# Optimization experiments

Hardware: AMD Instinct MI355X
Metric: run time of the kernel (lower is better)

## Reference

```python
import jax, jax.numpy as jnp
import numpy as np

AREA = 8  # area_size


def setup_inputs() -> dict:
    key = jax.random.key(0)
    ks = jax.random.split(key, 8)
    b, c, h, w = 4, 256, 252, 252
    cr = c // 8  # reduction=8
    return {
        "x": jax.random.normal(ks[0], (b, c, h, w), jnp.float32),
        "Wq": jax.random.normal(ks[1], (cr, c), jnp.float32) * 0.05,
        "bq": jax.random.normal(ks[2], (cr,), jnp.float32) * 0.05,
        "Wk": jax.random.normal(ks[3], (cr, c), jnp.float32) * 0.05,
        "bk": jax.random.normal(ks[4], (cr,), jnp.float32) * 0.05,
        "Wv": jax.random.normal(ks[5], (c, c), jnp.float32) * 0.05,
        "bv": jax.random.normal(ks[6], (c,), jnp.float32) * 0.05,
        "gamma": jax.random.normal(ks[7], (1,), jnp.float32) * 0.1,
    }


def _conv1x1(x, W, bias):
    # x: [b,c,h,w], W: [o,c] -> [b,o,h,w]
    return jnp.einsum('bchw,oc->bohw', x, W) + bias[None, :, None, None]


def reference(x, Wq, bq, Wk, bk, Wv, bv, gamma):
    a = AREA
    b, c, h, w = x.shape
    ph = ((h - 1) // a + 1) * a
    pw = ((w - 1) // a + 1) * a
    xp = jnp.pad(x, ((0, 0), (0, 0), (0, ph - h), (0, pw - w)))

    q = _conv1x1(xp, Wq, bq)  # [b,cr,ph,pw]
    k = _conv1x1(xp, Wk, bk)  # [b,cr,ph,pw]
    v = _conv1x1(xp, Wv, bv)  # [b,c,ph,pw]

    nh, nw = ph // a, pw // a

    def window(t):
        # [b,C,ph,pw] -> [b*nh*nw, C, a*a]
        C = t.shape[1]
        t = t.reshape(b, C, nh, a, nw, a)
        t = t.transpose(0, 2, 4, 1, 3, 5)
        return t.reshape(b * nh * nw, C, a * a)

    qw, kw, vw = window(q), window(k), window(v)

    # attn[n,i,j] = sum_c q[n,c,i] * k[n,c,j]; softmax over j
    attn = jax.nn.softmax(jnp.einsum('nci,ncj->nij', qw, kw), axis=2)
    # out[n,c,i] = sum_j v[n,c,j] * attn[i,j]
    out = jnp.einsum('ncj,nij->nci', vw, attn)

    out = out.reshape(b, nh, nw, c, a, a)
    out = out.transpose(0, 3, 1, 4, 2, 5).reshape(b, c, ph, pw)
    out = out[:, :, :h, :w]
    return gamma * out + x
```

## Files before the change

### kernel.cpp

```cpp
#include <hip/hip_runtime.h>


#define HH 252
#define WW 252
#define CC 256
#define HW (HH * WW)

typedef __attribute__((ext_vector_type(8))) short bf8;
typedef __attribute__((ext_vector_type(4))) float f32x4;

__device__ __forceinline__ short f2bf(float f) {
    union { float f; unsigned u; } v; v.f = f;
    unsigned u = v.u;
    unsigned r = (u + 0x7fffu + ((u >> 16) & 1u)) >> 16;
    return (short)r;
}

__global__ __launch_bounds__(256) void prep_weights(
        const float* __restrict__ Wq, const float* __restrict__ Wk,
        const float* __restrict__ Wv, short* __restrict__ wf) {
    int t = blockIdx.x * 256 + threadIdx.x;
    if (t >= 81920) return;
    const float* W; int off, base;
    if (t < 8192)       { W = Wq; off = t;         base = 0; }
    else if (t < 16384) { W = Wk; off = t - 8192;  base = 8192; }
    else                { W = Wv; off = t - 16384; base = 16384; }
    int j = off & 7, l = (off >> 3) & 63, tile = off >> 9;
    int kt = tile & 7, mt = tile >> 3;
    int m = mt * 16 + (l & 15);
    int k = kt * 32 + ((l >> 4) * 8) + j;
    wf[base + off] = f2bf(W[m * 256 + k]);
}

__global__ __launch_bounds__(256) void area_attn(
        const float* __restrict__ x, const short* __restrict__ wf,
        const float* __restrict__ bq, const float* __restrict__ bk,
        const float* __restrict__ bv, const float* __restrict__ gamma,
        float* __restrict__ out) {
    __shared__ short xs[64 * 264];
    __shared__ short qs[64 * 40];
    __shared__ short ks[64 * 40];
    __shared__ short ps[64 * 72];

    const int tid  = threadIdx.x;
    const int lane = tid & 63, wv = tid >> 6;
    const int l15  = lane & 15, quad = lane >> 4;

    const int bid  = blockIdx.x;
    const int xcd  = bid & 7;
    const int j    = bid >> 3;
    const int nx   = j & 31;
    const int grow = (j >> 5) * 8 + xcd;
    const int bimg = grow >> 5;
    const int ny   = grow & 31;
    const int hb = ny * 8, wb = nx * 8;
    const float* xb = x   + (size_t)bimg * CC * HW;
    float*       ob = out + (size_t)bimg * CC * HW;

    {
        int half = tid & 1, dy = (tid >> 1) & 7, cg = tid >> 4;
        int h = hb + dy;
        int w0 = wb + half * 4;
        bool inb = (h < HH) && (w0 < WW);
        const float* src = xb + (size_t)h * WW + w0;
        int p0 = dy * 8 + half * 4;
        for (int it = 0; it < 16; ++it) {
            int c = it * 16 + cg;
            float4 f;
            if (inb) f = *reinterpret_cast<const float4*>(src + (size_t)c * HW);
            else     f = make_float4(0.f, 0.f, 0.f, 0.f);
            xs[(p0 + 0) * 264 + c] = f2bf(f.x);
            xs[(p0 + 1) * 264 + c] = f2bf(f.y);
            xs[(p0 + 2) * 264 + c] = f2bf(f.z);
            xs[(p0 + 3) * 264 + c] = f2bf(f.w);
        }
    }
    __syncthreads();

    const f32x4 zero4 = {0.f, 0.f, 0.f, 0.f};

    {
        const bool isK = (wv >> 1) != 0;
        const int mt = wv & 1;
        const short* WF = wf + (isK ? 8192 : 0);
        const float* bias = isK ? bk : bq;
        f32x4 acc[4];
        for (int nt = 0; nt < 4; ++nt) acc[nt] = zero4;
        for (int kt = 0; kt < 8; ++kt) {
            bf8 a = *reinterpret_cast<const bf8*>(WF + ((mt * 8 + kt) * 64 + lane) * 8);
            for (int nt = 0; nt < 4; ++nt) {
                bf8 b = *reinterpret_cast<const bf8*>(
                    &xs[(nt * 16 + l15) * 264 + kt * 32 + quad * 8]);
                acc[nt] = __builtin_amdgcn_mfma_f32_16x16x32_bf16(a, b, acc[nt], 0, 0, 0);
            }
        }
        int cb = mt * 16 + quad * 4;
        float bi0 = bias[cb + 0], bi1 = bias[cb + 1];
        float bi2 = bias[cb + 2], bi3 = bias[cb + 3];
        short* dst = isK ? ks : qs;
        for (int nt = 0; nt < 4; ++nt) {
            int pos = nt * 16 + l15;
            short4 pk;
            pk.x = f2bf(acc[nt][0] + bi0);
            pk.y = f2bf(acc[nt][1] + bi1);
            pk.z = f2bf(acc[nt][2] + bi2);
            pk.w = f2bf(acc[nt][3] + bi3);
            *reinterpret_cast<short4*>(&dst[pos * 40 + cb]) = pk;
        }
    }

    f32x4 vacc[4][4];
    for (int mi = 0; mi < 4; ++mi)
        for (int nt = 0; nt < 4; ++nt) vacc[mi][nt] = zero4;
    {
        const short* WF = wf + 16384;
        for (int kt = 0; kt < 8; ++kt) {
            bf8 a[4];
            for (int mi = 0; mi < 4; ++mi)
                a[mi] = *reinterpret_cast<const bf8*>(
                    WF + (((wv * 4 + mi) * 8 + kt) * 64 + lane) * 8);
            for (int nt = 0; nt < 4; ++nt) {
                bf8 b = *reinterpret_cast<const bf8*>(
                    &xs[(nt * 16 + l15) * 264 + kt * 32 + quad * 8]);
                for (int mi = 0; mi < 4; ++mi)
                    vacc[mi][nt] = __builtin_amdgcn_mfma_f32_16x16x32_bf16(
                        a[mi], b, vacc[mi][nt], 0, 0, 0);
            }
        }
    }
    __syncthreads();

    for (int mi = 0; mi < 4; ++mi) {
        int cb = (wv * 4 + mi) * 16 + quad * 4;
        float b0 = bv[cb + 0], b1 = bv[cb + 1], b2 = bv[cb + 2], b3 = bv[cb + 3];
        for (int nt = 0; nt < 4; ++nt) {
            int pos = nt * 16 + l15;
            short4 pk;
            pk.x = f2bf(vacc[mi][nt][0] + b0);
            pk.y = f2bf(vacc[mi][nt][1] + b1);
            pk.z = f2bf(vacc[mi][nt][2] + b2);
            pk.w = f2bf(vacc[mi][nt][3] + b3);
            *reinterpret_cast<short4*>(&xs[pos * 264 + cb]) = pk;
        }
    }

    {
        f32x4 sacc[4];
        bf8 aq = *reinterpret_cast<const bf8*>(&qs[(wv * 16 + l15) * 40 + quad * 8]);
        for (int nt = 0; nt < 4; ++nt) {
            bf8 bk8 = *reinterpret_cast<const bf8*>(&ks[(nt * 16 + l15) * 40 + quad * 8]);
            sacc[nt] = __builtin_amdgcn_mfma_f32_16x16x32_bf16(aq, bk8, zero4, 0, 0, 0);
        }
        for (int r = 0; r < 4; ++r) {
            float mx = fmaxf(fmaxf(sacc[0][r], sacc[1][r]),
                             fmaxf(sacc[2][r], sacc[3][r]));
            for (int m = 1; m < 16; m <<= 1) mx = fmaxf(mx, __shfl_xor(mx, m, 64));
            float e0 = __expf(sacc[0][r] - mx);
            float e1 = __expf(sacc[1][r] - mx);
            float e2 = __expf(sacc[2][r] - mx);
            float e3 = __expf(sacc[3][r] - mx);
            float sum = e0 + e1 + e2 + e3;
            for (int m = 1; m < 16; m <<= 1) sum += __shfl_xor(sum, m, 64);
            float inv = 1.f / sum;
            int i = wv * 16 + quad * 4 + r;
            ps[i * 72 +  0 + l15] = f2bf(e0 * inv);
            ps[i * 72 + 16 + l15] = f2bf(e1 * inv);
            ps[i * 72 + 32 + l15] = f2bf(e2 * inv);
            ps[i * 72 + 48 + l15] = f2bf(e3 * inv);
        }
    }
    __syncthreads();

    f32x4 oacc[4][4];
    for (int mi = 0; mi < 4; ++mi)
        for (int nt = 0; nt < 4; ++nt) oacc[mi][nt] = zero4;
    for (int kt = 0; kt < 2; ++kt) {
        bf8 av[4];
        for (int mi = 0; mi < 4; ++mi) {
            int cidx = (wv * 4 + mi) * 16 + l15;
            bf8 a;
            for (int jj = 0; jj < 8; ++jj)
                a[jj] = xs[(kt * 32 + quad * 8 + jj) * 264 + cidx];
            av[mi] = a;
        }
        for (int nt = 0; nt < 4; ++nt) {
            bf8 bp = *reinterpret_cast<const bf8*>(
                &ps[(nt * 16 + l15) * 72 + kt * 32 + quad * 8]);
            for (int mi = 0; mi < 4; ++mi)
                oacc[mi][nt] = __builtin_amdgcn_mfma_f32_16x16x32_bf16(
                    av[mi], bp, oacc[mi][nt], 0, 0, 0);
        }
    }

    float g = gamma[0];
    for (int mi = 0; mi < 4; ++mi) {
        for (int r = 0; r < 4; ++r) {
            int c = (wv * 4 + mi) * 16 + quad * 4 + r;
            const float* xrow = xb + (size_t)c * HW;
            float*       orow = ob + (size_t)c * HW;
            for (int nt = 0; nt < 4; ++nt) {
                int pos = nt * 16 + l15;
                int h = hb + (pos >> 3), w = wb + (pos & 7);
                if (h < HH && w < WW) {
                    size_t idx = (size_t)h * WW + w;
                    orow[idx] = g * oacc[mi][nt][r] + xrow[idx];
                }
            }
        }
    }
}

extern "C" void kernel_launch(void* const* d_in, const int* in_sizes, int n_in,
                              void* d_out, int out_size, void* d_ws, size_t ws_size,
                              hipStream_t stream) {
    const float* x  = (const float*)d_in[0];
    const float* Wq = (const float*)d_in[1];
    const float* bq = (const float*)d_in[2];
    const float* Wk = (const float*)d_in[3];
    const float* bk = (const float*)d_in[4];
    const float* Wv = (const float*)d_in[5];
    const float* bv = (const float*)d_in[6];
    const float* gm = (const float*)d_in[7];
    short* wf = (short*)d_ws;

    prep_weights<<<320, 256, 0, stream>>>(Wq, Wk, Wv, wf);
    area_attn<<<4096, 256, 0, stream>>>(x, wf, bq, bk, bv, gm, (float*)d_out);
}
```

Baseline: 626.9 us.

## Swizzle shared-memory layouts, fuse Q/K/V projection loop, and raise occupancy

Replaces padded LDS arrays with XOR-swizzled layouts so the transposed V reads become vectorized bf8 loads instead of scalar gathers. It merges the Q/K and V projection loops to share the x fragments, stores V transposed (channel-major), and aliases the Q/K and P buffers to cut LDS use. It also adds a min-blocks launch bound of 4 and packs the bf16 conversions into wider stores. The cost is higher register pressure, since vacc and qacc are live together under the tighter launch bound, which could cause spills.

After: 685.7 us. 1.09x slower.

```diff
diff --git a/kernel.cpp b/kernel.cpp
--- a/kernel.cpp
+++ b/kernel.cpp
@@ -14,6 +14,28 @@
     unsigned u = v.u;
     unsigned r = (u + 0x7fffu + ((u >> 16) & 1u)) >> 16;
     return (short)r;
+}
+
+__device__ __forceinline__ unsigned pk2(float a, float b) {
+    return (unsigned)(unsigned short)f2bf(a) |
+           ((unsigned)(unsigned short)f2bf(b) << 16);
+}
+
+__device__ __forceinline__ int xaddr(int p, int c) {
+    int slot = (c >> 3) ^ ((p & 7) ^ ((p >> 3) & 7));
+    return p * 256 + (slot << 3) + (c & 7);
+}
+__device__ __forceinline__ int vaddr(int c, int p) {
+    int slot = ((p >> 3) ^ (c & 7)) & 7;
+    return c * 64 + (slot << 3) + (p & 7);
+}
+__device__ __forceinline__ int qaddr(int p, int cr) {
+    int slot = ((cr >> 3) ^ (p & 3)) & 3;
+    return p * 32 + (slot << 3) + (cr & 7);
+}
+__device__ __forceinline__ int paddr(int i, int j) {
+    int slot = ((j >> 3) ^ (i & 7)) & 7;
+    return i * 64 + (slot << 3) + (j & 7);
 }
 
 __global__ __launch_bounds__(256) void prep_weights(
@@ -32,15 +54,13 @@
     wf[base + off] = f2bf(W[m * 256 + k]);
 }
 
-__global__ __launch_bounds__(256) void area_attn(
+__global__ __launch_bounds__(256, 4) void area_attn(
         const float* __restrict__ x, const short* __restrict__ wf,
         const float* __restrict__ bq, const float* __restrict__ bk,
         const float* __restrict__ bv, const float* __restrict__ gamma,
         float* __restrict__ out) {
-    __shared__ short xs[64 * 264];
-    __shared__ short qs[64 * 40];
-    __shared__ short ks[64 * 40];
-    __shared__ short ps[64 * 72];
+    __shared__ short xs[16384];
+    __shared__ short qk[4096];
 
     const int tid  = threadIdx.x;
     const int lane = tid & 63, wv = tid >> 6;
@@ -48,109 +68,124 @@
 
     const int bid  = blockIdx.x;
     const int xcd  = bid & 7;
-    const int j    = bid >> 3;
-    const int nx   = j & 31;
-    const int grow = (j >> 5) * 8 + xcd;
+    const int jb   = bid >> 3;
+    const int nx   = jb & 31;
+    const int grow = (jb >> 5) * 8 + xcd;
     const int bimg = grow >> 5;
     const int ny   = grow & 31;
     const int hb = ny * 8, wb = nx * 8;
     const float* xb = x   + (size_t)bimg * CC * HW;
     float*       ob = out + (size_t)bimg * CC * HW;
 
-    {
-        int half = tid & 1, dy = (tid >> 1) & 7, cg = tid >> 4;
-        int h = hb + dy;
-        int w0 = wb + half * 4;
+    const f32x4 zero4 = {0.f, 0.f, 0.f, 0.f};
+
+    {
+        int s = tid & 15, cg = tid >> 4;
+        int h = hb + (s >> 1), w0 = wb + (s & 1) * 4;
         bool inb = (h < HH) && (w0 < WW);
         const float* src = xb + (size_t)h * WW + w0;
-        int p0 = dy * 8 + half * 4;
-        for (int it = 0; it < 16; ++it) {
-            int c = it * 16 + cg;
-            float4 f;
-            if (inb) f = *reinterpret_cast<const float4*>(src + (size_t)c * HW);
-            else     f = make_float4(0.f, 0.f, 0.f, 0.f);
-            xs[(p0 + 0) * 264 + c] = f2bf(f.x);
-            xs[(p0 + 1) * 264 + c] = f2bf(f.y);
-            xs[(p0 + 2) * 264 + c] = f2bf(f.z);
-            xs[(p0 + 3) * 264 + c] = f2bf(f.w);
-        }
-    }
-    __syncthreads();
-
-    const f32x4 zero4 = {0.f, 0.f, 0.f, 0.f};
-
-    {
-        const bool isK = (wv >> 1) != 0;
-        const int mt = wv & 1;
-        const short* WF = wf + (isK ? 8192 : 0);
+        int p0 = s * 4;
+        #pragma unroll
+        for (int it = 0; it < 4; ++it) {
+            int c0 = it * 64 + cg * 4;
+            float4 f[4];
+            #pragma unroll
+            for (int k = 0; k < 4; ++k) {
+                if (inb) f[k] = *reinterpret_cast<const float4*>(src + (size_t)(c0 + k) * HW);
+                else     f[k] = make_float4(0.f, 0.f, 0.f, 0.f);
+            }
+            #pragma unroll
+            for (int i = 0; i < 4; ++i) {
+                uint2 w2;
+                w2.x = pk2(((const float*)&f[0])[i], ((const float*)&f[1])[i]);
+                w2.y = pk2(((const float*)&f[2])[i], ((const float*)&f[3])[i]);
+                *reinterpret_cast<uint2*>(&xs[xaddr(p0 + i, c0)]) = w2;
+            }
+        }
+    }
+    __syncthreads();
+
+    const bool isK = (wv >> 1) != 0;
+    const int mt = wv & 1;
+    f32x4 qacc[4];
+    #pragma unroll
+    for (int nt = 0; nt < 4; ++nt) qacc[nt] = zero4;
+    f32x4 vacc[4][4];
+    #pragma unroll
+    for (int t = 0; t < 4; ++t)
+        #pragma unroll
+        for (int ni = 0; ni < 4; ++ni) vacc[t][ni] = zero4;
+    {
+        const short* WFqk = wf + (isK ? 8192 : 0);
+        #pragma unroll
+        for (int kt = 0; kt < 8; ++kt) {
+            bf8 xfr[4];
+            #pragma unroll
+            for (int t = 0; t < 4; ++t)
+                xfr[t] = *reinterpret_cast<const bf8*>(
+                    &xs[xaddr(t * 16 + l15, kt * 32 + quad * 8)]);
+            bf8 aw = *reinterpret_cast<const bf8*>(
+                WFqk + ((mt * 8 + kt) * 64 + lane) * 8);
+            #pragma unroll
+            for (int nt = 0; nt < 4; ++nt)
+                qacc[nt] = __builtin_amdgcn_mfma_f32_16x16x32_bf16(
+                    aw, xfr[nt], qacc[nt], 0, 0, 0);
+            #pragma unroll
+            for (int ni = 0; ni < 4; ++ni) {
+                bf8 bw = *reinterpret_cast<const bf8*>(
+                    wf + 16384 + (((wv * 4 + ni) * 8 + kt) * 64 + lane) * 8);
+                #pragma unroll
+                for (int t = 0; t < 4; ++t)
+                    vacc[t][ni] = __builtin_amdgcn_mfma_f32_16x16x32_bf16(
+                        xfr[t], bw, vacc[t][ni], 0, 0, 0);
+            }
+        }
+    }
+    {
+        int cb = mt * 16 + quad * 4;
         const float* bias = isK ? bk : bq;
-        f32x4 acc[4];
-        for (int nt = 0; nt < 4; ++nt) acc[nt] = zero4;
-        for (int kt = 0; kt < 8; ++kt) {
-            bf8 a = *reinterpret_cast<const bf8*>(WF + ((mt * 8 + kt) * 64 + lane) * 8);
-            for (int nt = 0; nt < 4; ++nt) {
-                bf8 b = *reinterpret_cast<const bf8*>(
-                    &xs[(nt * 16 + l15) * 264 + kt * 32 + quad * 8]);
-                acc[nt] = __builtin_amdgcn_mfma_f32_16x16x32_bf16(a, b, acc[nt], 0, 0, 0);
-            }
-        }
-        int cb = mt * 16 + quad * 4;
         float bi0 = bias[cb + 0], bi1 = bias[cb + 1];
         float bi2 = bias[cb + 2], bi3 = bias[cb + 3];
-        short* dst = isK ? ks : qs;
+        short* dst = isK ? (qk + 2048) : qk;
+        #pragma unroll
         for (int nt = 0; nt < 4; ++nt) {
             int pos = nt * 16 + l15;
-            short4 pk;
-            pk.x = f2bf(acc[nt][0] + bi0);
-            pk.y = f2bf(acc[nt][1] + bi1);
-            pk.z = f2bf(acc[nt][2] + bi2);
-            pk.w = f2bf(acc[nt][3] + bi3);
-            *reinterpret_cast<short4*>(&dst[pos * 40 + cb]) = pk;
-        }
-    }
-
-    f32x4 vacc[4][4];
-    for (int mi = 0; mi < 4; ++mi)
-        for (int nt = 0; nt < 4; ++nt) vacc[mi][nt] = zero4;
-    {
-        const short* WF = wf + 16384;
-        for (int kt = 0; kt < 8; ++kt) {
-            bf8 a[4];
-            for (int mi = 0; mi < 4; ++mi)
-                a[mi] = *reinterpret_cast<const bf8*>(
-                    WF + (((wv * 4 + mi) * 8 + kt) * 64 + lane) * 8);
-            for (int nt = 0; nt < 4; ++nt) {
-                bf8 b = *reinterpret_cast<const bf8*>(
-                    &xs[(nt * 16 + l15) * 264 + kt * 32 + quad * 8]);
-                for (int mi = 0; mi < 4; ++mi)
-                    vacc[mi][nt] = __builtin_amdgcn_mfma_f32_16x16x32_bf16(
-                        a[mi], b, vacc[mi][nt], 0, 0, 0);
-            }
-        }
-    }
-    __syncthreads();
-
-    for (int mi = 0; mi < 4; ++mi) {
-        int cb = (wv * 4 + mi) * 16 + quad * 4;
-        float b0 = bv[cb + 0], b1 = bv[cb + 1], b2 = bv[cb + 2], b3 = bv[cb + 3];
-        for (int nt = 0; nt < 4; ++nt) {
-            int pos = nt * 16 + l15;
-            short4 pk;
-            pk.x = f2bf(vacc[mi][nt][0] + b0);
-            pk.y = f2bf(vacc[mi][nt][1] + b1);
-            pk.z = f2bf(vacc[mi][nt][2] + b2);
-            pk.w = f2bf(vacc[mi][nt][3] + b3);
-            *reinterpret_cast<short4*>(&xs[pos * 264 + cb]) = pk;
-        }
-    }
+            uint2 w2;
+            w2.x = pk2(qacc[nt][0] + bi0, qacc[nt][1] + bi1);
+            w2.y = pk2(qacc[nt][2] + bi2, qacc[nt][3] + bi3);
+            *reinterpret_cast<uint2*>(&dst[qaddr(pos, cb)]) = w2;
+        }
+    }
+    __syncthreads();
+
+    #pragma unroll
+    for (int ni = 0; ni < 4; ++ni) {
+        int c = wv * 64 + ni * 16 + l15;
+        float bvc = bv[c];
+        #pragma unroll
+        for (int t = 0; t < 4; ++t) {
+            int p = t * 16 + quad * 4;
+            uint2 w2;
+            w2.x = pk2(vacc[t][ni][0] + bvc, vacc[t][ni][1] + bvc);
+            w2.y = pk2(vacc[t][ni][2] + bvc, vacc[t][ni][3] + bvc);
+            *reinterpret_cast<uint2*>(&xs[vaddr(c, p)]) = w2;
+        }
+    }
+    bf8 aq = *reinterpret_cast<const bf8*>(&qk[qaddr(wv * 16 + l15, quad * 8)]);
+    bf8 kb8[4];
+    #pragma unroll
+    for (int nt = 0; nt < 4; ++nt)
+        kb8[nt] = *reinterpret_cast<const bf8*>(
+            &qk[2048 + qaddr(nt * 16 + l15, quad * 8)]);
+    __syncthreads();
 
     {
         f32x4 sacc[4];
-        bf8 aq = *reinterpret_cast<const bf8*>(&qs[(wv * 16 + l15) * 40 + quad * 8]);
-        for (int nt = 0; nt < 4; ++nt) {
-            bf8 bk8 = *reinterpret_cast<const bf8*>(&ks[(nt * 16 + l15) * 40 + quad * 8]);
-            sacc[nt] = __builtin_amdgcn_mfma_f32_16x16x32_bf16(aq, bk8, zero4, 0, 0, 0);
-        }
+        #pragma unroll
+        for (int nt = 0; nt < 4; ++nt)
+            sacc[nt] = __builtin_amdgcn_mfma_f32_16x16x32_bf16(
+                aq, kb8[nt], zero4, 0, 0, 0);
+        #pragma unroll
         for (int r = 0; r < 4; ++r) {
             float mx = fmaxf(fmaxf(sacc[0][r], sacc[1][r]),
                              fmaxf(sacc[2][r], sacc[3][r]));
@@ -163,47 +198,52 @@
             for (int m = 1; m < 16; m <<= 1) sum += __shfl_xor(sum, m, 64);
             float inv = 1.f / sum;
             int i = wv * 16 + quad * 4 + r;
-            ps[i * 72 +  0 + l15] = f2bf(e0 * inv);
-            ps[i * 72 + 16 + l15] = f2bf(e1 * inv);
-            ps[i * 72 + 32 + l15] = f2bf(e2 * inv);
-            ps[i * 72 + 48 + l15] = f2bf(e3 * inv);
+            qk[paddr(i,  0 + l15)] = f2bf(e0 * inv);
+            qk[paddr(i, 16 + l15)] = f2bf(e1 * inv);
+            qk[paddr(i, 32 + l15)] = f2bf(e2 * inv);
+            qk[paddr(i, 48 + l15)] = f2bf(e3 * inv);
         }
     }
     __syncthreads();
 
     f32x4 oacc[4][4];
+    #pragma unroll
     for (int mi = 0; mi < 4; ++mi)
+        #pragma unroll
         for (int nt = 0; nt < 4; ++nt) oacc[mi][nt] = zero4;
+    #pragma unroll
     for (int kt = 0; kt < 2; ++kt) {
-        bf8 av[4];
-        for (int mi = 0; mi < 4; ++mi) {
-            int cidx = (wv * 4 + mi) * 16 + l15;
-            bf8 a;
-            for (int jj = 0; jj < 8; ++jj)
-                a[jj] = xs[(kt * 32 + quad * 8 + jj) * 264 + cidx];
-            av[mi] = a;
-        }
-        for (int nt = 0; nt < 4; ++nt) {
-            bf8 bp = *reinterpret_cast<const bf8*>(
-                &ps[(nt * 16 + l15) * 72 + kt * 32 + quad * 8]);
+        bf8 av[4], bp[4];
+        #pragma unroll
+        for (int mi = 0; mi < 4; ++mi)
+            av[mi] = *reinterpret_cast<const bf8*>(
+                &xs[vaddr((wv * 4 + mi) * 16 + l15, kt * 32 + quad * 8)]);
+        #pragma unroll
+        for (int nt = 0; nt < 4; ++nt)
+            bp[nt] = *reinterpret_cast<const bf8*>(
+                &qk[paddr(nt * 16 + l15, kt * 32 + quad * 8)]);
+        #pragma unroll
+        for (int nt = 0; nt < 4; ++nt)
+            #pragma unroll
             for (int mi = 0; mi < 4; ++mi)
                 oacc[mi][nt] = __builtin_amdgcn_mfma_f32_16x16x32_bf16(
-                    av[mi], bp, oacc[mi][nt], 0, 0, 0);
-        }
+                    av[mi], bp[nt], oacc[mi][nt], 0, 0, 0);
     }
 
     float g = gamma[0];
-    for (int mi = 0; mi < 4; ++mi) {
-        for (int r = 0; r < 4; ++r) {
-            int c = (wv * 4 + mi) * 16 + quad * 4 + r;
-            const float* xrow = xb + (size_t)c * HW;
-            float*       orow = ob + (size_t)c * HW;
-            for (int nt = 0; nt < 4; ++nt) {
-                int pos = nt * 16 + l15;
-                int h = hb + (pos >> 3), w = wb + (pos & 7);
-                if (h < HH && w < WW) {
-                    size_t idx = (size_t)h * WW + w;
-                    orow[idx] = g * oacc[mi][nt][r] + xrow[idx];
+    #pragma unroll
+    for (int nt = 0; nt < 4; ++nt) {
+        int pos = nt * 16 + l15;
+        int h = hb + (pos >> 3), w = wb + (pos & 7);
+        if (h < HH && w < WW) {
+            size_t idx = (size_t)h * WW + w;
+            #pragma unroll
+            for (int mi = 0; mi < 4; ++mi) {
+                int c0 = (wv * 4 + mi) * 16 + quad * 4;
+                #pragma unroll
+                for (int r = 0; r < 4; ++r) {
+                    size_t o = (size_t)(c0 + r) * HW + idx;
+                    ob[o] = g * oacc[mi][nt][r] + xb[o];
                 }
             }
         }
```
